# Kernel tuning notes

Measured on AMD Instinct MI355X. Metric: run time of the kernel, lower is better.

Reference implementation:

```python
import jax, jax.numpy as jnp
import numpy as np

NH, HD, MBS = 32, 64, 16   # num_heads, head_dim, mini_batch_size
BASE_LR = 1.0
ROPE_BASE = 10000.0
EPS = 1e-6


def _rotate_half(x):
    x1, x2 = jnp.split(x, 2, axis=-1)
    return jnp.concatenate((-x2, x1), axis=-1)


def _permute_qk(x):
    B, H, L, D = x.shape
    return x.reshape(B, H, L, D // 2, 2).swapaxes(-1, -2).reshape(B, H, L, D)


def _undo_permute_qk(x):
    B, H, L, D = x.shape
    return x.reshape(B, H, L, 2, D // 2).swapaxes(-1, -2).reshape(B, H, L, D)


def _ln_fwd(x, gamma, beta):
    mu = x.mean(-1, keepdims=True)
    var = x.var(-1, keepdims=True)
    return gamma * ((x - mu) / jnp.sqrt(var + EPS)) + beta


def _ln_fused_l2_bwd(x, target, gamma, beta):
    # grad of 0.5*||LN(x) - target||^2 wrt x, fused
    D = x.shape[-1]
    mu = x.mean(-1, keepdims=True)
    std = jnp.sqrt(x.var(-1, keepdims=True) + EPS)
    x_hat = (x - mu) / std
    y = gamma * x_hat + beta
    g = (y - target) * gamma
    return (D * g - g.sum(-1, keepdims=True) - x_hat * (g * x_hat).sum(-1, keepdims=True)) / (D * std)


def setup_inputs() -> dict:
    key = jax.random.key(0)
    ks = jax.random.split(key, 8)
    B, L, C, OUT = 4, 2048, 2048, 768
    s = 0.02
    return {
        "hidden_states": jax.random.normal(ks[0], (B, L, C), jnp.float32),
        "position_ids": jnp.broadcast_to(jnp.arange(L, dtype=jnp.int32)[None], (B, L)),
        "Wq": jax.random.normal(ks[1], (C, C), jnp.float32) * s,
        "Wk": jax.random.normal(ks[2], (C, C), jnp.float32) * s,
        "Wv": jax.random.normal(ks[3], (C, C), jnp.float32) * s,
        "Wo": jax.random.normal(ks[4], (C, OUT), jnp.float32) * s,
        "W1": jax.random.normal(ks[5], (NH, HD, HD), jnp.float32) * s,
        "b1": jnp.zeros((NH, 1, HD), jnp.float32),
        "ttt_lr_weight": jax.random.normal(ks[6], (NH, 1, C), jnp.float32) * s,
        "ttt_lr_bias": jnp.zeros((NH, 1), jnp.float32),
        "learnable_token_idx": jnp.zeros((MBS,), jnp.float32),
        "ttt_norm_weight": jnp.ones((NH, HD), jnp.float32),
        "ttt_norm_bias": jnp.zeros((NH, HD), jnp.float32),
        "post_norm_weight": jnp.ones((C,), jnp.float32),
        "post_norm_bias": jnp.zeros((C,), jnp.float32),
    }


def reference(hidden_states, position_ids, Wq, Wk, Wv, Wo, W1, b1,
              ttt_lr_weight, ttt_lr_bias, learnable_token_idx,
              ttt_norm_weight, ttt_norm_bias, post_norm_weight, post_norm_bias):
    B, L, C = hidden_states.shape
    NM = L // MBS
    # QKV projections -> [B, NH, L, HD]
    XQ = (hidden_states @ Wq).reshape(B, L, NH, HD).transpose(0, 2, 1, 3)
    XK = (hidden_states @ Wk).reshape(B, L, NH, HD).transpose(0, 2, 1, 3)
    XV = (hidden_states @ Wv).reshape(B, L, NH, HD).transpose(0, 2, 1, 3)
    # RoPE on positions modulo the mini-batch size
    pos = (position_ids % MBS).astype(jnp.float32)  # [B, L]
    inv_freq = 1.0 / (ROPE_BASE ** (jnp.arange(0, HD, 2, dtype=jnp.float32) / HD))
    freqs = pos[..., None] * inv_freq               # [B, L, HD/2]
    emb = jnp.concatenate((freqs, freqs), axis=-1)  # [B, L, HD]
    cos = jnp.cos(emb)[:, None]                     # [B, 1, L, HD]
    sin = jnp.sin(emb)[:, None]
    XQ, XK = _permute_qk(XQ), _permute_qk(XK)
    XQ = XQ * cos + _rotate_half(XQ) * sin
    XK = XK * cos + _rotate_half(XK) * sin
    XQ, XK = _undo_permute_qk(XQ), _undo_permute_qk(XK)
    # reshape into mini-batches: [B, NH, NM, K, HD]
    X = hidden_states.reshape(B, NM, MBS, C)
    XQ = XQ.reshape(B, NH, NM, MBS, HD)
    XK = XK.reshape(B, NH, NM, MBS, HD)
    XV = XV.reshape(B, NH, NM, MBS, HD)
    # eta: per-token learnable LR gate
    ttt_lr = jax.nn.sigmoid(
        jnp.einsum('bnkc,hdc->bhnkd', X, ttt_lr_weight)
        + ttt_lr_bias.reshape(1, NH, 1, 1, 1))              # [B,NH,NM,K,1]
    ttt_lr_eta = BASE_LR * ttt_lr.transpose(0, 1, 2, 4, 3) / HD  # [B,NH,NM,1,K]
    token_idx = jnp.clip(1.0 / jnp.arange(1, MBS + 1, dtype=jnp.float32)
                         + learnable_token_idx, 0.0, None)
    token_eta = token_idx.reshape(1, 1, 1, MBS, 1)
    eta = token_eta * ttt_lr_eta                            # [B,NH,NM,K,K]
    # TTT-Linear dual-form mini-batch scan
    ln_w = ttt_norm_weight.reshape(1, NH, 1, HD)
    ln_b = ttt_norm_bias.reshape(1, NH, 1, HD)
    W1_0 = jnp.broadcast_to(W1[None], (B, NH, HD, HD))
    b1_0 = jnp.broadcast_to(b1[None], (B, NH, 1, HD))
    tril = jnp.tril(jnp.ones((MBS, MBS), hidden_states.dtype))

    def step(carry, xs):
        W1_s, b1_s = carry
        xq, xk, xv, eta_m = xs                 # [B,NH,K,HD], eta_m [B,NH,K,K]
        Z1 = xk @ W1_s + b1_s
        target = xv - xk
        grad = _ln_fused_l2_bwd(Z1, target, ln_w, ln_b)
        Attn = tril * (xq @ xk.swapaxes(-1, -2))
        b1_bar = b1_s - (tril * eta_m) @ grad
        Z1_bar = xq @ W1_s - (eta_m * Attn) @ grad + b1_bar
        last_eta = eta_m[:, :, -1, :, None]    # [B,NH,K,1]
        W1_new = W1_s - (last_eta * xk).swapaxes(-1, -2) @ grad
        b1_new = b1_s - jnp.sum(last_eta * grad, axis=-2, keepdims=True)
        out = xq + _ln_fwd(Z1_bar, ln_w, ln_b)
        return (W1_new, b1_new), out

    xs = (XQ.transpose(2, 0, 1, 3, 4), XK.transpose(2, 0, 1, 3, 4),
          XV.transpose(2, 0, 1, 3, 4), eta.transpose(2, 0, 1, 3, 4))
    _, outs = jax.lax.scan(step, (W1_0, b1_0), xs)   # [NM,B,NH,K,HD]
    out = outs.transpose(1, 2, 0, 3, 4).reshape(B, NH, L, HD)
    out = out.transpose(0, 2, 1, 3).reshape(B, L, C)
    # post LayerNorm (eps 1e-6) and output projection
    mu = out.mean(-1, keepdims=True)
    var = out.var(-1, keepdims=True)
    out = (out - mu) / jnp.sqrt(var + EPS) * post_norm_weight + post_norm_bias
    return out @ Wo
```

## Files before the change

kernel.cpp:

```cpp
#include <hip/hip_runtime.h>
#include <cstddef>
#include <cstdint>

#define B_DIM   4
#define L_SEQ   2048
#define C_DIM   2048
#define OUT_DIM 768
#define NHEADS  32
#define HDIM    64
#define MBS_    16
#define NMINI   128
#define EPS_    1e-6f

typedef _Float16 half8 __attribute__((ext_vector_type(8)));
typedef _Float16 half4 __attribute__((ext_vector_type(4)));
typedef float floatx4 __attribute__((ext_vector_type(4)));

__device__ __forceinline__ void glds16(const void* g, void* l) {
    __builtin_amdgcn_global_load_lds(
        (const __attribute__((address_space(1))) uint32_t*)g,
        (__attribute__((address_space(3))) uint32_t*)l, 16, 0, 0);
}

__device__ __forceinline__ void split8(const float4 a, const float4 b,
                                       half8& hi, half8& lo) {
    const float x[8] = {a.x, a.y, a.z, a.w, b.x, b.y, b.z, b.w};
#pragma unroll
    for (int e = 0; e < 8; e++) {
        const _Float16 h = (_Float16)x[e];
        hi[e] = h;
        lo[e] = (_Float16)(x[e] - (float)h);
    }
}

__device__ __forceinline__ void split4(const float4 a, half4& hi, half4& lo) {
    const float x[4] = {a.x, a.y, a.z, a.w};
#pragma unroll
    for (int e = 0; e < 4; e++) {
        const _Float16 h = (_Float16)x[e];
        hi[e] = h;
        lo[e] = (_Float16)(x[e] - (float)h);
    }
}

__device__ __forceinline__ uint32_t pack_hl(float v) {
    const _Float16 h = (_Float16)v;
    const _Float16 l = (_Float16)(v - (float)h);
    union { _Float16 f[2]; uint32_t u; } p;
    p.f[0] = h; p.f[1] = l;
    return p.u;
}

__device__ __forceinline__ half8 pairswap(half8 v) {
    union { half8 h; uint32_t u[4]; } a, b;
    a.h = v;
#pragma unroll
    for (int e = 0; e < 4; e++) b.u[e] = (a.u[e] >> 16) | (a.u[e] << 16);
    return b.h;
}

template<int CTRL>
__device__ __forceinline__ float dpp_add(float v) {
    const int x = __builtin_amdgcn_update_dpp(0, __float_as_int(v), CTRL, 0xF, 0xF, false);
    return v + __int_as_float(x);
}
__device__ __forceinline__ float red16(float v) {
    v = dpp_add<0xB1>(v);
    v = dpp_add<0x4E>(v);
    v = dpp_add<0x124>(v);
    v = dpp_add<0x128>(v);
    return v;
}

__device__ __forceinline__ void bar_lgkm() {
    asm volatile("s_waitcnt lgkmcnt(0)\n\ts_barrier" ::: "memory");
}

__global__ __launch_bounds__(256)
void gemm_af32(const float* __restrict__ A,
               const _Float16* __restrict__ Bhi, const _Float16* __restrict__ Blo,
               float* __restrict__ Cout, int mode, int doRope)
{
    __shared__ __align__(16) float    sA[4096];
    __shared__ __align__(16) _Float16 sBhi[4096];
    __shared__ __align__(16) _Float16 sBlo[4096];
    const int tid = threadIdx.x;
    const int m0 = blockIdx.y * 128, n0 = blockIdx.x * 128;
    const int K = 2048;

    size_t gA[4]; float* lA[4];
#pragma unroll
    for (int I = 0; I < 4; I++) {
        const int c = I * 256 + tid;
        const int row = c >> 3, seg = (c & 7) ^ (row & 7);
        gA[I] = (size_t)(m0 + row) * K + seg * 4;
        lA[I] = &sA[c * 4];
    }
    size_t gB[2]; _Float16 *lBh[2], *lBl[2];
#pragma unroll
    for (int I = 0; I < 2; I++) {
        const int c = I * 256 + tid;
        const int row = c >> 2, seg = (c & 3) ^ ((row >> 1) & 3);
        gB[I] = (size_t)(n0 + row) * K + seg * 8;
        lBh[I] = &sBhi[c * 8];
        lBl[I] = &sBlo[c * 8];
    }

    const int lane = tid & 63, quad = lane >> 4, lc = lane & 15;
    const int wv = tid >> 6, wm = wv & 1, wn = wv >> 1;
    int offA0[4], offA1[4], offB[4];
#pragma unroll
    for (int i = 0; i < 4; i++) {
        const int rA = wm * 64 + i * 16 + lc;
        offA0[i] = (rA * 8 + ((2 * quad)     ^ (rA & 7))) * 4;
        offA1[i] = (rA * 8 + ((2 * quad + 1) ^ (rA & 7))) * 4;
    }
#pragma unroll
    for (int j = 0; j < 4; j++) {
        const int rB = wn * 64 + j * 16 + lc;
        offB[j] = (rB * 4 + (quad ^ ((rB >> 1) & 3))) * 8;
    }

    floatx4 acc[4][4];
#pragma unroll
    for (int i = 0; i < 4; i++)
#pragma unroll
        for (int j = 0; j < 4; j++) acc[i][j] = (floatx4)0.0f;

    for (int k0 = 0; k0 < K; k0 += 32) {
        __syncthreads();
#pragma unroll
        for (int I = 0; I < 4; I++) glds16(A + gA[I] + k0, lA[I]);
#pragma unroll
        for (int I = 0; I < 2; I++) {
            glds16(Bhi + gB[I] + k0, lBh[I]);
            glds16(Blo + gB[I] + k0, lBl[I]);
        }
        __syncthreads();

        half8 ah[4], al[4], bh[4], bl[4];
#pragma unroll
        for (int i = 0; i < 4; i++) {
            const float4 va = *(const float4*)&sA[offA0[i]];
            const float4 vb = *(const float4*)&sA[offA1[i]];
            split8(va, vb, ah[i], al[i]);
        }
#pragma unroll
        for (int j = 0; j < 4; j++) {
            bh[j] = *(const half8*)&sBhi[offB[j]];
            bl[j] = *(const half8*)&sBlo[offB[j]];
        }
#pragma unroll
        for (int i = 0; i < 4; i++)
#pragma unroll
            for (int j = 0; j < 4; j++) {
                acc[i][j] = __builtin_amdgcn_mfma_f32_16x16x32_f16(ah[i], bh[j], acc[i][j], 0, 0, 0);
                acc[i][j] = __builtin_amdgcn_mfma_f32_16x16x32_f16(ah[i], bl[j], acc[i][j], 0, 0, 0);
                acc[i][j] = __builtin_amdgcn_mfma_f32_16x16x32_f16(al[i], bh[j], acc[i][j], 0, 0, 0);
            }
    }

    float cs[4][4], sn[4][4];
    if (doRope) {
#pragma unroll
        for (int j = 0; j < 4; j++) {
            const int ii = ((j * 16 + lc) & 63) >> 1;
            const float invf = expf(-(float)ii * 0.28782313662425574f);
#pragma unroll
            for (int r = 0; r < 4; r++) {
                const float ang = (float)(quad * 4 + r) * invf;
                sincosf(ang, &sn[j][r], &cs[j][r]);
            }
        }
    }
    const int oddcol = lc & 1;
#pragma unroll
    for (int i = 0; i < 4; i++) {
#pragma unroll
        for (int j = 0; j < 4; j++) {
            floatx4 v = acc[i][j];
            if (doRope) {
#pragma unroll
                for (int r = 0; r < 4; r++) {
                    const float partner = __shfl_xor(v[r], 1);
                    v[r] = v[r] * cs[j][r] + partner * (oddcol ? sn[j][r] : -sn[j][r]);
                }
            }
            const int n = n0 + wn * 64 + j * 16 + lc;
            if (mode == 0) {
                const int h = (n >> 6) & 31, d = n & 63;
#pragma unroll
                for (int r = 0; r < 4; r++) {
                    const int m = m0 + wm * 64 + i * 16 + quad * 4 + r;
                    const int b = m >> 11, li = m & 2047;
                    Cout[((size_t)(b * 32 + h) * 2048 + li) * 64 + d] = v[r];
                }
            } else {
#pragma unroll
                for (int r = 0; r < 4; r++) {
                    const int m = m0 + wm * 64 + i * 16 + quad * 4 + r;
                    Cout[(size_t)m * OUT_DIM + n] = v[r];
                }
            }
        }
    }
}

__global__ __launch_bounds__(256)
void wtrans_kernel(const float* __restrict__ W, _Float16* __restrict__ BThi,
                   _Float16* __restrict__ BTlo, int Nw)
{
    __shared__ float tile[32][33];
    const int t = threadIdx.x, tx = t & 31, ty = t >> 5;
    const int n0 = blockIdx.x * 32, k0 = blockIdx.y * 32;
    const int K = 2048;
#pragma unroll
    for (int r = 0; r < 4; r++)
        tile[ty + r * 8][tx] = W[(size_t)(k0 + ty + r * 8) * Nw + n0 + tx];
    __syncthreads();
#pragma unroll
    for (int r = 0; r < 4; r++) {
        const float val = tile[tx][ty + r * 8];
        const _Float16 hh = (_Float16)val;
        const size_t o = (size_t)(n0 + ty + r * 8) * K + k0 + tx;
        BThi[o] = hh;
        BTlo[o] = (_Float16)(val - (float)hh);
    }
}

__global__ __launch_bounds__(256)
void lr_kernel(const float* __restrict__ hidden, const float* __restrict__ wlr,
               const float* __restrict__ lr_bias, float* __restrict__ lrs)
{
    __shared__ float sRow[2048];
    __shared__ float sPart[32][9];
    const int m = blockIdx.x;
    const int t = threadIdx.x;
    const float* row = hidden + (size_t)m * C_DIM;
#pragma unroll
    for (int j = 0; j < 8; j++) sRow[t + j * 256] = row[t + j * 256];
    __syncthreads();
    const int h = t >> 3, p = t & 7;
    const float* w = wlr + (size_t)h * C_DIM;
    float s = 0.0f;
#pragma unroll 8
    for (int k = 0; k < 64; k++) {
        const int c = k * 32 + p * 4;
        const float4 a = *(const float4*)(sRow + c);
        const float4 b = *(const float4*)(w + c);
        s += a.x * b.x + a.y * b.y + a.z * b.z + a.w * b.w;
    }
    sPart[h][p] = s;
    __syncthreads();
    if (t < 32) {
        float v = 0.0f;
#pragma unroll
        for (int p2 = 0; p2 < 8; p2++) v += sPart[t][p2];
        v += lr_bias[t];
        const float sig = 1.0f / (1.0f + expf(-v));
        lrs[((size_t)(m >> 11) * NHEADS + t) * L_SEQ + (m & 2047)] = sig;
    }
}

__global__ __launch_bounds__(256, 1)
void scan_mfma(const float* __restrict__ XQ, const float* __restrict__ XK,
               float* __restrict__ XVo, const float* __restrict__ LRS,
               const float* __restrict__ W1i, const float* __restrict__ b1i,
               const float* __restrict__ lt, const float* __restrict__ lnw,
               const float* __restrict__ lnb)
{
    __shared__ __align__(16) _Float16 sXqH[1024], sXqL[1024];
    __shared__ __align__(16) _Float16 sXkH[1024], sXkL[1024];
    __shared__ __align__(16) float    sTgt[16 * 68];
    __shared__ __align__(16) float    sXq32[2][16 * 68];
    __shared__ __align__(16) _Float16 sW1H[4096], sW1L[4096];
    __shared__ __align__(16) uint32_t sKT[64 * 20];
    __shared__ __align__(16) uint32_t sCf[16 * 20];
    __shared__ __align__(16) float sRedA[16 * 36];
    __shared__ __align__(16) float sRedC[16 * 12];
    __shared__ __align__(16) float sEta[16];
    __shared__ float sB1[64];

    const int bh = blockIdx.x, h = bh & 31;
    const int t = threadIdx.x;
    const int lane = t & 63, q = lane >> 4, lc = lane & 15;
    const int w = t >> 6;
    const int col = w * 16 + lc;
    const int iRow = t >> 4;
    const int m = t & 15;

    if (t < 64) sB1[t] = b1i[h * 64 + t];

    float w1s[4][4];
#pragma unroll
    for (int t4 = 0; t4 < 4; t4++)
#pragma unroll
        for (int r = 0; r < 4; r++) {
            const float v = W1i[h * 4096 + (16 * t4 + lc) * 64 + (16 * w + 4 * q + r)];
            w1s[t4][r] = v;
            const int nn = 16 * w + 4 * q + r, k = 16 * t4 + lc;
            const int off = nn * 64 + ((((k >> 3) ^ (nn & 7)) << 3) | (k & 7));
            const _Float16 hh = (_Float16)v;
            sW1H[off] = hh; sW1L[off] = (_Float16)(v - (float)hh);
        }

    const float gamC = lnw[h * 64 + col], betC = lnb[h * 64 + col];
    const float g2c = gamC * gamC;
    float sumG2 = 0.0f;
#pragma unroll
    for (int d0 = 0; d0 < 16; d0++) {
        const float4 gv = *(const float4*)(lnw + h * 64 + d0 * 4);
        sumG2 += gv.x * gv.x + gv.y * gv.y + gv.z * gv.z + gv.w * gv.w;
    }
    float tokR[4];
#pragma unroll
    for (int r = 0; r < 4; r++)
        tokR[r] = fmaxf(1.0f / (float)(4 * q + r + 1) + lt[4 * q + r], 0.0f);
    const float tok15 = fmaxf(1.0f / 16.0f + lt[15], 0.0f);

    __syncthreads();

    const size_t base = (size_t)bh * L_SEQ * HDIM;
    const float* xq_g = XQ + base;
    const float* xk_g = XK + base;
    float* xv_g = XVo + base;
    const float* lr_g = LRS + (size_t)bh * L_SEQ;

    float4 cq = *(const float4*)(xq_g + t * 4);
    float4 ck = *(const float4*)(xk_g + t * 4);
    float4 cv = *(const float4*)(xv_g + t * 4);
    float clr = lr_g[m];

    const int rw = 16 * w + lc;
    const int stOff = iRow * 64 + ((((m >> 1) ^ (iRow & 7)) << 3) | ((m & 1) << 2));
    const int gkm = (m ^ (m >> 2)) & 3;
    const int ktWb = 4 * (w ^ gkm) + q;

    for (int n = 0; n < NMINI; n++) {
        const int buf = n & 1;
        {
            half4 hq, lq, hk, lk;
            split4(cq, hq, lq);
            split4(ck, hk, lk);
            *(half4*)&sXqH[stOff] = hq;
            *(half4*)&sXqL[stOff] = lq;
            *(half4*)&sXkH[stOff] = hk;
            *(half4*)&sXkL[stOff] = lk;
            const float4 tg = make_float4(cv.x - ck.x, cv.y - ck.y,
                                          cv.z - ck.z, cv.w - ck.w);
            *(float4*)&sTgt[iRow * 68 + m * 4] = tg;
            *(float4*)&sXq32[buf][iRow * 68 + m * 4] = cq;
            const float kvv[4] = {ck.x, ck.y, ck.z, ck.w};
#pragma unroll
            for (int i2 = 0; i2 < 4; i2++)
                sKT[(4 * m + i2) * 20 + ktWb] = pack_hl(kvv[i2]);
        }
        if (t < 16) sEta[t] = clr * (1.0f / 64.0f);
        const int np = (n + 1) & (NMINI - 1);
        const float4 nq = *(const float4*)(xq_g + np * 1024 + t * 4);
        const float4 nk = *(const float4*)(xk_g + np * 1024 + t * 4);
        const float4 nv = *(const float4*)(xv_g + np * 1024 + t * 4);
        const float nlr = lr_g[np * 16 + m];
        bar_lgkm();

        const float b1c = sB1[col];
        const float4 ev = *(const float4*)&sEta[4 * q];
        const float evv[4] = {ev.x, ev.y, ev.z, ev.w};

        half8 qh[2], ql[2], kh[2], kl[2], wh[2], wl[2];
#pragma unroll
        for (int f = 0; f < 2; f++) {
            const int cx = ((4 * f + q) ^ (lc & 7)) << 3;
            qh[f] = *(const half8*)&sXqH[lc * 64 + cx];
            ql[f] = *(const half8*)&sXqL[lc * 64 + cx];
            kh[f] = *(const half8*)&sXkH[lc * 64 + cx];
            kl[f] = *(const half8*)&sXkL[lc * 64 + cx];
            const int cw = ((4 * f + q) ^ (rw & 7)) << 3;
            wh[f] = *(const half8*)&sW1H[rw * 64 + cw];
            wl[f] = *(const half8*)&sW1L[rw * 64 + cw];
        }

        floatx4 z1a = (floatx4)0.0f, zba = (floatx4)0.0f, at = (floatx4)0.0f;
#pragma unroll
        for (int f = 0; f < 2; f++) {
            z1a = __builtin_amdgcn_mfma_f32_16x16x32_f16(kh[f], wh[f], z1a, 0, 0, 0);
            z1a = __builtin_amdgcn_mfma_f32_16x16x32_f16(kh[f], wl[f], z1a, 0, 0, 0);
            z1a = __builtin_amdgcn_mfma_f32_16x16x32_f16(kl[f], wh[f], z1a, 0, 0, 0);
            zba = __builtin_amdgcn_mfma_f32_16x16x32_f16(qh[f], wh[f], zba, 0, 0, 0);
            zba = __builtin_amdgcn_mfma_f32_16x16x32_f16(qh[f], wl[f], zba, 0, 0, 0);
            zba = __builtin_amdgcn_mfma_f32_16x16x32_f16(ql[f], wh[f], zba, 0, 0, 0);
        }
        if (w == 0) {
            const float etaLC = sEta[lc];
#pragma unroll
            for (int f = 0; f < 2; f++) {
                at = __builtin_amdgcn_mfma_f32_16x16x32_f16(qh[f], kh[f], at, 0, 0, 0);
                at = __builtin_amdgcn_mfma_f32_16x16x32_f16(qh[f], kl[f], at, 0, 0, 0);
                at = __builtin_amdgcn_mfma_f32_16x16x32_f16(ql[f], kh[f], at, 0, 0, 0);
            }
#pragma unroll
            for (int r = 0; r < 4; r++) {
                const int i = 4 * q + r;
                const float cfv = (lc <= i) ? -tokR[r] * etaLC * (at[r] + 1.0f) : 0.0f;
                sCf[i * 20 + 4 * ((lc >> 2) ^ q) + (lc & 3)] = pack_hl(cfv);
            }
        }

        float z[4], cE[4];
        float sz[4], szz[4], sgz[4], sgzz[4], sc[4], scz[4];
#pragma unroll
        for (int r = 0; r < 4; r++) {
            const int row = 4 * q + r;
            z[r] = z1a[r] + b1c;
            const float tgt = sTgt[row * 68 + col];
            cE[r] = gamC * (betC - tgt);
            const float zz = z[r] * z[r];
            sz[r]   = red16(z[r]);
            szz[r]  = red16(zz);
            sgz[r]  = red16(g2c * z[r]);
            sgzz[r] = red16(g2c * zz);
            sc[r]   = red16(cE[r]);
            scz[r]  = red16(cE[r] * z[r]);
        }
        if (lc == 0) {
#pragma unroll
            for (int r = 0; r < 4; r++) {
                const int rb = (4 * q + r) * 36;
                sRedA[rb + 0  + w] = sz[r];
                sRedA[rb + 4  + w] = szz[r];
                sRedA[rb + 8  + w] = sgz[r];
                sRedA[rb + 12 + w] = sgzz[r];
                sRedA[rb + 16 + w] = sc[r];
                sRedA[rb + 20 + w] = scz[r];
            }
        }
        bar_lgkm();

        half8 ktp[4];
#pragma unroll
        for (int t4 = 0; t4 < 4; t4++) {
            const int gkr = ((lc >> 2) ^ t4) & 3;
            ktp[t4] = *(const half8*)&sKT[(16 * t4 + lc) * 20 + 4 * (q ^ gkr)];
        }
        const half8 cfp = *(const half8*)&sCf[lc * 20 + 4 * (q ^ (lc >> 2))];

        float gr[4];
#pragma unroll
        for (int r = 0; r < 4; r++) {
            const int rb = (4 * q + r) * 36;
            const float4 a0 = *(const float4*)&sRedA[rb + 0];
            const float4 a1 = *(const float4*)&sRedA[rb + 4];
            const float4 a2 = *(const float4*)&sRedA[rb + 8];
            const float4 a3 = *(const float4*)&sRedA[rb + 12];
            const float4 a4 = *(const float4*)&sRedA[rb + 16];
            const float4 a5 = *(const float4*)&sRedA[rb + 20];
            const float Sz   = a0.x + a0.y + a0.z + a0.w;
            const float Szz  = a1.x + a1.y + a1.z + a1.w;
            const float Sgz  = a2.x + a2.y + a2.z + a2.w;
            const float Sgzz = a3.x + a3.y + a3.z + a3.w;
            const float Sc   = a4.x + a4.y + a4.z + a4.w;
            const float Scz  = a5.x + a5.y + a5.z + a5.w;
            const float mu  = Sz * (1.0f / 64.0f);
            const float ex2 = Szz * (1.0f / 64.0f);
            const float rs  = rsqrtf(ex2 - mu * mu + EPS_);
            const float G1 = rs * (Sgz - mu * sumG2) + Sc;
            const float G2 = rs * rs * (Sgzz - 2.0f * mu * Sgz + mu * mu * sumG2)
                           + rs * (Scz - mu * Sc);
            const float xh = (z[r] - mu) * rs;
            const float g  = g2c * xh + cE[r];
            gr[r] = (64.0f * g - G1 - xh * G2) * rs * (1.0f / 64.0f);
        }

        half8 gf, gfl;
#pragma unroll
        for (int r = 0; r < 4; r++) {
            const _Float16 h0 = (_Float16)gr[r];
            gf[2 * r]     = h0;
            gf[2 * r + 1] = (_Float16)(gr[r] - (float)h0);
            const float gl = gr[r] * (tok15 * evv[r]);
            const _Float16 h1 = (_Float16)gl;
            gfl[2 * r]     = h1;
            gfl[2 * r + 1] = (_Float16)(gl - (float)h1);
        }
        const half8 gfs  = pairswap(gf);
        const half8 gfls = pairswap(gfl);

        zba = __builtin_amdgcn_mfma_f32_16x16x32_f16(cfp, gf,  zba, 0, 0, 0);
        zba = __builtin_amdgcn_mfma_f32_16x16x32_f16(cfp, gfs, zba, 0, 0, 0);
#pragma unroll
        for (int t4 = 0; t4 < 4; t4++) {
            floatx4 up = (floatx4)0.0f;
            up = __builtin_amdgcn_mfma_f32_16x16x32_f16(gfl,  ktp[t4], up, 0, 0, 0);
            up = __builtin_amdgcn_mfma_f32_16x16x32_f16(gfls, ktp[t4], up, 0, 0, 0);
#pragma unroll
            for (int r = 0; r < 4; r++) w1s[t4][r] -= up[r];
        }

        float z2[4], p1[4], p2[4];
#pragma unroll
        for (int r = 0; r < 4; r++) {
            z2[r] = zba[r] + b1c;
            p1[r] = red16(z2[r]);
            p2[r] = red16(z2[r] * z2[r]);
        }
        if (lc == 0)
#pragma unroll
            for (int r = 0; r < 4; r++) {
                const int rb = (4 * q + r) * 12;
                sRedC[rb + w]     = p1[r];
                sRedC[rb + 4 + w] = p2[r];
            }

        {
            float p = gr[0] * evv[0] + gr[1] * evv[1] + gr[2] * evv[2] + gr[3] * evv[3];
            p += __shfl_xor(p, 16);
            p += __shfl_xor(p, 32);
            if (q == 0) sB1[col] -= tok15 * p;
        }
#pragma unroll
        for (int t4 = 0; t4 < 4; t4++)
#pragma unroll
            for (int r = 0; r < 4; r++) {
                const int nn = 16 * w + 4 * q + r, k = 16 * t4 + lc;
                const int off = nn * 64 + ((((k >> 3) ^ (nn & 7)) << 3) | (k & 7));
                const float v = w1s[t4][r];
                const _Float16 hh = (_Float16)v;
                sW1H[off] = hh; sW1L[off] = (_Float16)(v - (float)hh);
            }
        bar_lgkm();

#pragma unroll
        for (int r = 0; r < 4; r++) {
            const int row = 4 * q + r;
            const float4 a = *(const float4*)&sRedC[row * 12];
            const float4 b = *(const float4*)&sRedC[row * 12 + 4];
            const float mu  = (a.x + a.y + a.z + a.w) * (1.0f / 64.0f);
            const float ex2 = (b.x + b.y + b.z + b.w) * (1.0f / 64.0f);
            const float rs  = rsqrtf(ex2 - mu * mu + EPS_);
            const float xqv = sXq32[buf][row * 68 + col];
            xv_g[n * 1024 + row * 64 + col] = xqv + gamC * ((z2[r] - mu) * rs) + betC;
        }
        cq = nq; ck = nk; cv = nv; clr = nlr;
    }
}

__global__ __launch_bounds__(256)
void postln_kernel(const float* __restrict__ Ob, const float* __restrict__ pnw,
                   const float* __restrict__ pnb, float* __restrict__ XN)
{
    const int m = blockIdx.x;
    const int b = m >> 11, l = m & 2047;
    const int t = threadIdx.x;
    float v[8];
    float s1 = 0.0f, s2 = 0.0f;
    const float* bas = Ob + (size_t)b * NHEADS * L_SEQ * HDIM + (size_t)l * HDIM;
#pragma unroll
    for (int j = 0; j < 8; j++) {
        const int c = t + j * 256;
        const int hh = c >> 6, d = c & 63;
        const float x = bas[(size_t)hh * (L_SEQ * HDIM) + d];
        v[j] = x; s1 += x; s2 += x * x;
    }
#pragma unroll
    for (int o = 1; o < 64; o <<= 1) { s1 += __shfl_xor(s1, o); s2 += __shfl_xor(s2, o); }
    __shared__ float r1[4], r2[4];
    const int w = t >> 6;
    if ((t & 63) == 0) { r1[w] = s1; r2[w] = s2; }
    __syncthreads();
    s1 = r1[0] + r1[1] + r1[2] + r1[3];
    s2 = r2[0] + r2[1] + r2[2] + r2[3];
    const float mu = s1 * (1.0f / 2048.0f);
    const float var = s2 * (1.0f / 2048.0f) - mu * mu;
    const float rstd = rsqrtf(var + EPS_);
    float* o = XN + (size_t)m * C_DIM;
#pragma unroll
    for (int j = 0; j < 8; j++) {
        const int c = t + j * 256;
        o[c] = (v[j] - mu) * rstd * pnw[c] + pnb[c];
    }
}

extern "C" void kernel_launch(void* const* d_in, const int* in_sizes, int n_in,
                              void* d_out, int out_size, void* d_ws, size_t ws_size,
                              hipStream_t stream)
{
    (void)in_sizes; (void)n_in; (void)out_size;
    const float* hidden  = (const float*)d_in[0];
    const float* Wq      = (const float*)d_in[2];
    const float* Wk      = (const float*)d_in[3];
    const float* Wv      = (const float*)d_in[4];
    const float* Wo      = (const float*)d_in[5];
    const float* W1      = (const float*)d_in[6];
    const float* b1      = (const float*)d_in[7];
    const float* wlr     = (const float*)d_in[8];
    const float* lr_bias = (const float*)d_in[9];
    const float* lt      = (const float*)d_in[10];
    const float* lnw     = (const float*)d_in[11];
    const float* lnb     = (const float*)d_in[12];
    const float* pnw     = (const float*)d_in[13];
    const float* pnb     = (const float*)d_in[14];

    const size_t TEN = (size_t)B_DIM * NHEADS * L_SEQ * HDIM;
    float* XQ  = (float*)d_ws;
    float* XK  = XQ + TEN;
    float* XVo = XK + TEN;
    float* LRS = XVo + TEN;
    const dim3 blk(256);

    _Float16* BThi = (_Float16*)d_out;
    _Float16* BTlo = BThi + (size_t)C_DIM * C_DIM;

    lr_kernel<<<dim3(B_DIM * L_SEQ), blk, 0, stream>>>(hidden, wlr, lr_bias, LRS);

    const float* Wmats[3] = {Wq, Wk, Wv};
    float* outs[3] = {XQ, XK, XVo};
    for (int p = 0; p < 3; p++) {
        wtrans_kernel<<<dim3(64, 64), blk, 0, stream>>>(Wmats[p], BThi, BTlo, C_DIM);
        gemm_af32<<<dim3(16, 64), blk, 0, stream>>>(hidden, BThi, BTlo,
                                                    outs[p], 0, (p < 2) ? 1 : 0);
    }
    scan_mfma<<<dim3(B_DIM * NHEADS), blk, 0, stream>>>(XQ, XK, XVo, LRS,
                                                        W1, b1, lt, lnw, lnb);
    float* XN = XQ;
    _Float16* WThi = (_Float16*)XK;
    _Float16* WTlo = WThi + (size_t)OUT_DIM * C_DIM;
    postln_kernel<<<dim3(B_DIM * L_SEQ), blk, 0, stream>>>(XVo, pnw, pnb, XN);
    wtrans_kernel<<<dim3(24, 64), blk, 0, stream>>>(Wo, WThi, WTlo, OUT_DIM);
    gemm_af32<<<dim3(6, 64), blk, 0, stream>>>(XN, WThi, WTlo,
                                               (float*)d_out, 1, 0);
}
```

Before: 1.423 ms.

## Pre-split GEMM A operand into fp16 hi/lo and swizzle workgroup order

A new kernel converts the fp32 hidden states into fp16 hi/lo halves once, up front. The QKV GEMMs then load ready-made halves instead of re-splitting the same A tile inside every n-tile workgroup. The post-LayerNorm kernel is vectorised and writes its output directly as hi/lo halves for the output projection. A workgroup index remap groups blocks for better L2 reuse. In exchange it adds an extra pass over the input, extra workspace, and a fallback path that depends on workspace size.

```diff
diff --git a/kernel.cpp b/kernel.cpp
--- a/kernel.cpp
+++ b/kernel.cpp
@@ -77,24 +77,66 @@
 }
 
 __global__ __launch_bounds__(256)
-void gemm_af32(const float* __restrict__ A,
-               const _Float16* __restrict__ Bhi, const _Float16* __restrict__ Blo,
-               float* __restrict__ Cout, int mode, int doRope)
+void asplit_kernel(const float* __restrict__ A, _Float16* __restrict__ Ahi,
+                   _Float16* __restrict__ Alo)
 {
-    __shared__ __align__(16) float    sA[4096];
+    const size_t idx = ((size_t)blockIdx.x * 256 + threadIdx.x) * 16;
+    half8 h0, l0, h1, l1;
+    {
+        const float4 a = *(const float4*)(A + idx);
+        const float4 b = *(const float4*)(A + idx + 4);
+        split8(a, b, h0, l0);
+    }
+    {
+        const float4 a = *(const float4*)(A + idx + 8);
+        const float4 b = *(const float4*)(A + idx + 12);
+        split8(a, b, h1, l1);
+    }
+    *(half8*)(Ahi + idx)     = h0;
+    *(half8*)(Ahi + idx + 8) = h1;
+    *(half8*)(Alo + idx)     = l0;
+    *(half8*)(Alo + idx + 8) = l1;
+}
+
+template<int APRE>
+__global__ __launch_bounds__(256)
+void gemm_t(const float* __restrict__ A32,
+            const _Float16* __restrict__ Ahi, const _Float16* __restrict__ Alo,
+            const _Float16* __restrict__ Bhi, const _Float16* __restrict__ Blo,
+            float* __restrict__ Cout, int mode, int doRope)
+{
+    __shared__ __align__(16) float    sA[APRE ? 1 : 4096];
+    __shared__ __align__(16) _Float16 sAh[APRE ? 4096 : 1];
+    __shared__ __align__(16) _Float16 sAl[APRE ? 4096 : 1];
     __shared__ __align__(16) _Float16 sBhi[4096];
     __shared__ __align__(16) _Float16 sBlo[4096];
     const int tid = threadIdx.x;
-    const int m0 = blockIdx.y * 128, n0 = blockIdx.x * 128;
+    const int nwg = gridDim.x * gridDim.y;
+    int lin = blockIdx.y * gridDim.x + blockIdx.x;
+    lin = (lin & 7) * (nwg >> 3) + (lin >> 3);
+    const int m0 = (lin / gridDim.x) * 128;
+    const int n0 = (lin % gridDim.x) * 128;
     const int K = 2048;
 
     size_t gA[4]; float* lA[4];
-#pragma unroll
-    for (int I = 0; I < 4; I++) {
-        const int c = I * 256 + tid;
-        const int row = c >> 3, seg = (c & 7) ^ (row & 7);
-        gA[I] = (size_t)(m0 + row) * K + seg * 4;
-        lA[I] = &sA[c * 4];
+    size_t gAs[2]; _Float16 *lAh[2], *lAl[2];
+    if constexpr (!APRE) {
+#pragma unroll
+        for (int I = 0; I < 4; I++) {
+            const int c = I * 256 + tid;
+            const int row = c >> 3, seg = (c & 7) ^ (row & 7);
+            gA[I] = (size_t)(m0 + row) * K + seg * 4;
+            lA[I] = &sA[c * 4];
+        }
+    } else {
+#pragma unroll
+        for (int I = 0; I < 2; I++) {
+            const int c = I * 256 + tid;
+            const int row = c >> 2, seg = (c & 3) ^ ((row >> 1) & 3);
+            gAs[I] = (size_t)(m0 + row) * K + seg * 8;
+            lAh[I] = &sAh[c * 8];
+            lAl[I] = &sAl[c * 8];
+        }
     }
     size_t gB[2]; _Float16 *lBh[2], *lBl[2];
 #pragma unroll
@@ -108,12 +150,16 @@
 
     const int lane = tid & 63, quad = lane >> 4, lc = lane & 15;
     const int wv = tid >> 6, wm = wv & 1, wn = wv >> 1;
-    int offA0[4], offA1[4], offB[4];
+    int offA0[4], offA1[4], offAp[4], offB[4];
 #pragma unroll
     for (int i = 0; i < 4; i++) {
         const int rA = wm * 64 + i * 16 + lc;
-        offA0[i] = (rA * 8 + ((2 * quad)     ^ (rA & 7))) * 4;
-        offA1[i] = (rA * 8 + ((2 * quad + 1) ^ (rA & 7))) * 4;
+        if constexpr (!APRE) {
+            offA0[i] = (rA * 8 + ((2 * quad)     ^ (rA & 7))) * 4;
+            offA1[i] = (rA * 8 + ((2 * quad + 1) ^ (rA & 7))) * 4;
+        } else {
+            offAp[i] = (rA * 4 + (quad ^ ((rA >> 1) & 3))) * 8;
+        }
     }
 #pragma unroll
     for (int j = 0; j < 4; j++) {
@@ -129,8 +175,16 @@
 
     for (int k0 = 0; k0 < K; k0 += 32) {
         __syncthreads();
-#pragma unroll
-        for (int I = 0; I < 4; I++) glds16(A + gA[I] + k0, lA[I]);
+        if constexpr (!APRE) {
+#pragma unroll
+            for (int I = 0; I < 4; I++) glds16(A32 + gA[I] + k0, lA[I]);
+        } else {
+#pragma unroll
+            for (int I = 0; I < 2; I++) {
+                glds16(Ahi + gAs[I] + k0, lAh[I]);
+                glds16(Alo + gAs[I] + k0, lAl[I]);
+            }
+        }
 #pragma unroll
         for (int I = 0; I < 2; I++) {
             glds16(Bhi + gB[I] + k0, lBh[I]);
@@ -141,9 +195,14 @@
         half8 ah[4], al[4], bh[4], bl[4];
 #pragma unroll
         for (int i = 0; i < 4; i++) {
-            const float4 va = *(const float4*)&sA[offA0[i]];
-            const float4 vb = *(const float4*)&sA[offA1[i]];
-            split8(va, vb, ah[i], al[i]);
+            if constexpr (!APRE) {
+                const float4 va = *(const float4*)&sA[offA0[i]];
+                const float4 vb = *(const float4*)&sA[offA1[i]];
+                split8(va, vb, ah[i], al[i]);
+            } else {
+                ah[i] = *(const half8*)&sAh[offAp[i]];
+                al[i] = *(const half8*)&sAl[offAp[i]];
+            }
         }
 #pragma unroll
         for (int j = 0; j < 4; j++) {
@@ -546,21 +605,26 @@
 
 __global__ __launch_bounds__(256)
 void postln_kernel(const float* __restrict__ Ob, const float* __restrict__ pnw,
-                   const float* __restrict__ pnb, float* __restrict__ XN)
+                   const float* __restrict__ pnb, _Float16* __restrict__ XNhi,
+                   _Float16* __restrict__ XNlo)
 {
     const int m = blockIdx.x;
     const int b = m >> 11, l = m & 2047;
     const int t = threadIdx.x;
     float v[8];
     float s1 = 0.0f, s2 = 0.0f;
-    const float* bas = Ob + (size_t)b * NHEADS * L_SEQ * HDIM + (size_t)l * HDIM;
-#pragma unroll
-    for (int j = 0; j < 8; j++) {
-        const int c = t + j * 256;
-        const int hh = c >> 6, d = c & 63;
-        const float x = bas[(size_t)hh * (L_SEQ * HDIM) + d];
-        v[j] = x; s1 += x; s2 += x * x;
-    }
+    const int c0 = t * 8;
+    const int hh = c0 >> 6, d0 = c0 & 63;
+    const float* bas = Ob + (size_t)b * NHEADS * L_SEQ * HDIM + (size_t)l * HDIM
+                     + (size_t)hh * (L_SEQ * HDIM) + d0;
+    {
+        const float4 va = *(const float4*)(bas);
+        const float4 vb = *(const float4*)(bas + 4);
+        v[0] = va.x; v[1] = va.y; v[2] = va.z; v[3] = va.w;
+        v[4] = vb.x; v[5] = vb.y; v[6] = vb.z; v[7] = vb.w;
+    }
+#pragma unroll
+    for (int j = 0; j < 8; j++) { s1 += v[j]; s2 += v[j] * v[j]; }
 #pragma unroll
     for (int o = 1; o < 64; o <<= 1) { s1 += __shfl_xor(s1, o); s2 += __shfl_xor(s2, o); }
     __shared__ float r1[4], r2[4];
@@ -572,12 +636,16 @@
     const float mu = s1 * (1.0f / 2048.0f);
     const float var = s2 * (1.0f / 2048.0f) - mu * mu;
     const float rstd = rsqrtf(var + EPS_);
-    float* o = XN + (size_t)m * C_DIM;
+    half8 oh, ol;
 #pragma unroll
     for (int j = 0; j < 8; j++) {
-        const int c = t + j * 256;
-        o[c] = (v[j] - mu) * rstd * pnw[c] + pnb[c];
-    }
+        const float y = (v[j] - mu) * rstd * pnw[c0 + j] + pnb[c0 + j];
+        const _Float16 hy = (_Float16)y;
+        oh[j] = hy;
+        ol[j] = (_Float16)(y - (float)hy);
+    }
+    *(half8*)(XNhi + (size_t)m * C_DIM + c0) = oh;
+    *(half8*)(XNlo + (size_t)m * C_DIM + c0) = ol;
 }
 
 extern "C" void kernel_launch(void* const* d_in, const int* in_sizes, int n_in,
@@ -605,27 +673,42 @@
     float* XK  = XQ + TEN;
     float* XVo = XK + TEN;
     float* LRS = XVo + TEN;
+    _Float16* Ahi = (_Float16*)(LRS + 262144);
+    _Float16* Alo = Ahi + TEN;
+    const size_t needBytes = (3 * TEN + 262144) * 4 + TEN * 4;
+    const int useAsplit = (ws_size >= needBytes) ? 1 : 0;
     const dim3 blk(256);
 
     _Float16* BThi = (_Float16*)d_out;
     _Float16* BTlo = BThi + (size_t)C_DIM * C_DIM;
 
     lr_kernel<<<dim3(B_DIM * L_SEQ), blk, 0, stream>>>(hidden, wlr, lr_bias, LRS);
+    if (useAsplit)
+        asplit_kernel<<<dim3(4096), blk, 0, stream>>>(hidden, Ahi, Alo);
 
     const float* Wmats[3] = {Wq, Wk, Wv};
     float* outs[3] = {XQ, XK, XVo};
     for (int p = 0; p < 3; p++) {
         wtrans_kernel<<<dim3(64, 64), blk, 0, stream>>>(Wmats[p], BThi, BTlo, C_DIM);
-        gemm_af32<<<dim3(16, 64), blk, 0, stream>>>(hidden, BThi, BTlo,
-                                                    outs[p], 0, (p < 2) ? 1 : 0);
+        if (useAsplit)
+            gemm_t<1><<<dim3(16, 64), blk, 0, stream>>>(nullptr, Ahi, Alo,
+                                                        BThi, BTlo, outs[p],
+                                                        0, (p < 2) ? 1 : 0);
+        else
+            gemm_t<0><<<dim3(16, 64), blk, 0, stream>>>(hidden, nullptr, nullptr,
+                                                        BThi, BTlo, outs[p],
+                                                        0, (p < 2) ? 1 : 0);
     }
     scan_mfma<<<dim3(B_DIM * NHEADS), blk, 0, stream>>>(XQ, XK, XVo, LRS,
                                                         W1, b1, lt, lnw, lnb);
-    float* XN = XQ;
-    _Float16* WThi = (_Float16*)XK;
+    _Float16* XNhi = (_Float16*)XQ;
+    _Float16* XNlo = XNhi + TEN;
+    _Float16* WThi = (_Float16*)XVo;
+    WThi = (_Float16*)XK;
     _Float16* WTlo = WThi + (size_t)OUT_DIM * C_DIM;
-    postln_kernel<<<dim3(B_DIM * L_SEQ), blk, 0, stream>>>(XVo, pnw, pnb, XN);
+    postln_kernel<<<dim3(B_DIM * L_SEQ), blk, 0, stream>>>(XVo, pnw, pnb,
+                                                           XNhi, XNlo);
     wtrans_kernel<<<dim3(24, 64), blk, 0, stream>>>(Wo, WThi, WTlo, OUT_DIM);
-    gemm_af32<<<dim3(6, 64), blk, 0, stream>>>(XN, WThi, WTlo,
-                                               (float*)d_out, 1, 0);
-}
+    gemm_t<1><<<dim3(6, 64), blk, 0, stream>>>(nullptr, XNhi, XNlo,
+                                               WThi, WTlo, (float*)d_out, 1, 0);
+}
```

After: 1.401 ms. Within noise of the previous version (-1.6%).
